# Optimization experiments

Hardware: AMD Instinct MI355X
Metric: run time of the kernel (lower is better)

Reference implementation:

```python
import jax, jax.numpy as jnp
import numpy as np

C = 384; NH = 12; HD = C // NH; MLP = int(C * 4.0)
B = 8; T = 12; N = 256; BT = B * T
EPS = 1e-6


def _ln(x):
    # LayerNorm without affine, eps=1e-6
    mu = jnp.mean(x, axis=-1, keepdims=True)
    var = jnp.mean(jnp.square(x - mu), axis=-1, keepdims=True)
    return (x - mu) / jnp.sqrt(var + EPS)


def _attention(x, wqkv, bqkv, wproj, bproj, bias=None):
    b, n, c = x.shape
    qkv = (x @ wqkv.T + bqkv).reshape(b, n, 3, NH, HD)
    q = qkv[:, :, 0].transpose(0, 2, 1, 3)  # [b,h,n,d]
    k = qkv[:, :, 1].transpose(0, 2, 1, 3)
    v = qkv[:, :, 2].transpose(0, 2, 1, 3)
    attn = jnp.einsum('bhnd,bhmd->bhnm', q, k) * (HD ** -0.5)
    if bias is not None:
        attn = attn + bias
    attn = jax.nn.softmax(attn, axis=-1)
    out = jnp.einsum('bhnm,bhmd->bhnd', attn, v).transpose(0, 2, 1, 3).reshape(b, n, c)
    return out @ wproj.T + bproj, attn


def setup_inputs() -> dict:
    key = jax.random.key(0)
    ks = jax.random.split(key, 20)
    s = 0.02
    inp = {
        'x': jax.random.normal(ks[0], (BT, N, C), jnp.float32),
        'c': jax.random.normal(ks[1], (BT, C), jnp.float32),
        'rel_pos_bias': jax.random.normal(ks[2], (1, NH, N, N), jnp.float32) * s,
        'w_adaln': jax.random.normal(ks[3], (9 * C, C), jnp.float32) * s,
        'b_adaln': jnp.zeros((9 * C,), jnp.float32),
        'wqkv_s': jax.random.normal(ks[4], (3 * C, C), jnp.float32) * s,
        'bqkv_s': jnp.zeros((3 * C,), jnp.float32),
        'wproj_s': jax.random.normal(ks[5], (C, C), jnp.float32) * s,
        'bproj_s': jnp.zeros((C,), jnp.float32),
        'wqkv_t': jax.random.normal(ks[6], (3 * C, C), jnp.float32) * s,
        'bqkv_t': jnp.zeros((3 * C,), jnp.float32),
        'wproj_t': jax.random.normal(ks[7], (C, C), jnp.float32) * s,
        'bproj_t': jnp.zeros((C,), jnp.float32),
        'w1': jax.random.normal(ks[8], (MLP, C), jnp.float32) * s,
        'b1': jnp.zeros((MLP,), jnp.float32),
        'w2': jax.random.normal(ks[9], (C, MLP), jnp.float32) * s,
        'b2': jnp.zeros((C,), jnp.float32),
        'T_pred': T,
    }
    return inp


def reference(x, c, rel_pos_bias, w_adaln, b_adaln, wqkv_s, bqkv_s, wproj_s, bproj_s,
              wqkv_t, bqkv_t, wproj_t, bproj_t, w1, b1, w2, b2, T_pred):
    mod = jax.nn.silu(c) @ w_adaln.T + b_adaln  # [BT, 9C]
    (shift_s, scale_s, gate_s, shift_t, scale_t, gate_t,
     shift_mlp, scale_mlp, gate_mlp) = jnp.split(mod, 9, axis=1)

    # spatial attention with adaLN modulate + gate
    x_mod = _ln(x) * (1 + scale_s[:, None]) + shift_s[:, None]
    x_s, attn_map = _attention(x_mod, wqkv_s, bqkv_s, wproj_s, bproj_s, bias=rel_pos_bias)
    x = x + gate_s[:, None] * x_s

    if T_pred > 1:
        bt, n, cdim = x.shape
        b = bt // T_pred
        xt = x.reshape(b, T_pred, n, cdim).transpose(0, 2, 1, 3).reshape(b * n, T_pred, cdim)
        sc = scale_t.reshape(b, 1, T_pred, cdim)
        sh = shift_t.reshape(b, 1, T_pred, cdim)
        gt = gate_t.reshape(b, 1, T_pred, cdim)
        norm_t = _ln(xt).reshape(b, n, T_pred, cdim)
        mod_t = (norm_t * (1 + sc) + sh).reshape(b * n, T_pred, cdim)
        x_t, _ = _attention(mod_t, wqkv_t, bqkv_t, wproj_t, bproj_t)
        x_t = (x_t.reshape(b, n, T_pred, cdim) * gt).transpose(0, 2, 1, 3).reshape(bt, n, cdim)
        x = x + x_t

    # gated MLP with exact (erf) GELU, matching nn.GELU default
    h = _ln(x) * (1 + scale_mlp[:, None]) + shift_mlp[:, None]
    h = jax.nn.gelu(h @ w1.T + b1, approximate=False) @ w2.T + b2
    x = x + gate_mlp[:, None] * h
    return (x, attn_map)
```

## Files before the change

### kernel.cpp

```cpp
#include <hip/hip_runtime.h>
#include <hip/hip_bf16.h>
#include <math.h>

typedef __bf16 bf16;
typedef __bf16 bf16x8 __attribute__((ext_vector_type(8)));
typedef __bf16 bf16x4 __attribute__((ext_vector_type(4)));
typedef float  f32x4  __attribute__((ext_vector_type(4)));

#define C_    384
#define NH_   12
#define HD_   32
#define MLP_  1536
#define B_    8
#define T_    12
#define N_    256
#define BT_   96
#define M_    24576
#define NINE_C 3456
#define QKV_  1152

#define GLOAD16(gptr, lptr)                                                \
  __builtin_amdgcn_global_load_lds(                                       \
      (const __attribute__((address_space(1))) void*)(gptr),              \
      (__attribute__((address_space(3))) void*)(lptr), 16, 0, 0)

__device__ __forceinline__ float wave_sum(float v) {
#pragma unroll
  for (int o = 32; o > 0; o >>= 1) v += __shfl_xor(v, o, 64);
  return v;
}

template <typename TO> __device__ __forceinline__ TO to_out(float v);
template <> __device__ __forceinline__ float to_out<float>(float v) { return v; }
template <> __device__ __forceinline__ bf16  to_out<bf16>(float v)  { return (bf16)v; }

struct F2BArgs {
  const float* src[8];
  bf16* dst[8];
  int n4[8];
};
__global__ __launch_bounds__(256) void k_f2b_all(F2BArgs a) {
  const int seg = blockIdx.y;
  const int i = blockIdx.x * 256 + threadIdx.x;
  if (i >= a.n4[seg]) return;
  if (seg == 7) {
    bf16x4 o;
    if (i < 9216) {
      float4 v = ((const float4*)a.src[7])[i];
      o[0] = (bf16)(v.x / (1.f + __expf(-v.x)));
      o[1] = (bf16)(v.y / (1.f + __expf(-v.y)));
      o[2] = (bf16)(v.z / (1.f + __expf(-v.z)));
      o[3] = (bf16)(v.w / (1.f + __expf(-v.w)));
    } else {
      o[0] = o[1] = o[2] = o[3] = (bf16)0.f;
    }
    ((bf16x4*)a.dst[7])[i] = o;
    return;
  }
  float4 v = ((const float4*)a.src[seg])[i];
  bf16x4 o;
  o[0] = (bf16)v.x; o[1] = (bf16)v.y; o[2] = (bf16)v.z; o[3] = (bf16)v.w;
  ((bf16x4*)a.dst[seg])[i] = o;
}

__global__ __launch_bounds__(256) void k_ln_mod(const float* __restrict__ x,
                                                const float* __restrict__ mod,
                                                bf16* __restrict__ out,
                                                int shift_chunk, int scale_chunk) {
  const int wave = threadIdx.x >> 6, lane = threadIdx.x & 63;
  const int r = blockIdx.x * 4 + wave;
  const float* xr = x + (size_t)r * C_;
  float2 v[3];
  float s = 0.f, ss = 0.f;
#pragma unroll
  for (int e = 0; e < 3; ++e) {
    v[e] = *(const float2*)&xr[lane * 2 + 128 * e];
    s += v[e].x + v[e].y;
    ss += v[e].x * v[e].x + v[e].y * v[e].y;
  }
  s = wave_sum(s); ss = wave_sum(ss);
  const float mean = s * (1.f / C_);
  const float var  = ss * (1.f / C_) - mean * mean;
  const float rs   = rsqrtf(var + 1e-6f);
  const int bt = r >> 8;
  const float* sh = mod + (size_t)bt * NINE_C + shift_chunk * C_;
  const float* sc = mod + (size_t)bt * NINE_C + scale_chunk * C_;
  bf16* orow = out + (size_t)r * C_;
#pragma unroll
  for (int e = 0; e < 3; ++e) {
    int cc = lane * 2 + 128 * e;
    float2 s2 = *(const float2*)&sc[cc];
    float2 h2 = *(const float2*)&sh[cc];
    union { bf16 b[2]; unsigned u; } pk;
    pk.b[0] = (bf16)((v[e].x - mean) * rs * (1.f + s2.x) + h2.x);
    pk.b[1] = (bf16)((v[e].y - mean) * rs * (1.f + s2.y) + h2.y);
    *(unsigned*)&orow[cc] = pk.u;
  }
}

template <typename TO, int EPI>
__global__ __launch_bounds__(256) void mfma_gemm(const bf16* __restrict__ A,
                                                 const bf16* __restrict__ W,
                                                 const float* __restrict__ bias,
                                                 TO* __restrict__ out,
                                                 int M, int N, int K,
                                                 const float* __restrict__ base,
                                                 const float* __restrict__ mod,
                                                 int gc, int ntx) {
  __shared__ bf16 As[128 * 64];
  __shared__ bf16 Bs[128 * 64];
  const int tid = threadIdx.x;
  const int w = tid >> 6, l = tid & 63;
  const int nwg = gridDim.x;
  const int q8 = nwg >> 3, r8 = nwg & 7;
  const int xcd = blockIdx.x & 7, idx = blockIdx.x >> 3;
  const int t = (xcd < r8 ? xcd * (q8 + 1) : r8 * (q8 + 1) + (xcd - r8) * q8) + idx;
  const int m0 = (t / ntx) * 128, n0 = (t % ntx) * 128;
  const int wr = w >> 1, wc = w & 1;
  f32x4 acc[4][4];
#pragma unroll
  for (int mi = 0; mi < 4; ++mi)
#pragma unroll
    for (int nj = 0; nj < 4; ++nj) acc[mi][nj] = (f32x4){0.f, 0.f, 0.f, 0.f};

  const int srow8 = l >> 3;
  const int c8    = l & 7;

  for (int k0 = 0; k0 < K; k0 += 64) {
#pragma unroll
    for (int i = 0; i < 4; ++i) {
      int row = w * 32 + i * 8 + srow8;
      int sc = c8 ^ (row & 7);
      GLOAD16(A + (size_t)(m0 + row) * K + k0 + sc * 8,
              (char*)As + (w * 32 + i * 8) * 128);
      GLOAD16(W + (size_t)(n0 + row) * K + k0 + sc * 8,
              (char*)Bs + (w * 32 + i * 8) * 128);
    }
    __syncthreads();
#pragma unroll
    for (int kt = 0; kt < 2; ++kt) {
      bf16x8 a[4], b[4];
      const int cc = kt * 4 + (l >> 4);
#pragma unroll
      for (int mi = 0; mi < 4; ++mi) {
        int row = wr * 64 + mi * 16 + (l & 15);
        a[mi] = *(const bf16x8*)((const char*)As + row * 128 + ((cc ^ (row & 7)) << 4));
      }
#pragma unroll
      for (int nj = 0; nj < 4; ++nj) {
        int row = wc * 64 + nj * 16 + (l & 15);
        b[nj] = *(const bf16x8*)((const char*)Bs + row * 128 + ((cc ^ (row & 7)) << 4));
      }
#pragma unroll
      for (int mi = 0; mi < 4; ++mi)
#pragma unroll
        for (int nj = 0; nj < 4; ++nj)
          acc[mi][nj] = __builtin_amdgcn_mfma_f32_16x16x32_bf16(a[mi], b[nj], acc[mi][nj], 0, 0, 0);
    }
    __syncthreads();
  }
  const int btc = m0 >> 8;
#pragma unroll
  for (int nj = 0; nj < 4; ++nj) {
    int col = n0 + wc * 64 + nj * 16 + (l & 15);
    float bv = bias[col];
    float gv = 0.f;
    if (EPI == 2 || EPI == 4) gv = mod[(size_t)btc * NINE_C + gc * C_ + col];
#pragma unroll
    for (int mi = 0; mi < 4; ++mi) {
#pragma unroll
      for (int q = 0; q < 4; ++q) {
        int rrow = m0 + wr * 64 + mi * 16 + (l >> 4) * 4 + q;
        float v = acc[mi][nj][q] + bv;
        if (EPI == 0) {
          out[(size_t)rrow * N + col] = to_out<TO>(v);
        } else if (EPI == 1) {
          v = 0.5f * v * (1.f + erff(v * 0.70710678118654752f));
          out[(size_t)rrow * N + col] = to_out<TO>(v);
        } else if (EPI == 2) {
          ((float*)out)[(size_t)rrow * N + col] =
              base[(size_t)rrow * N + col] + gv * v;
        } else {
          float o = base[(size_t)rrow * N + col] + gv * v;
          __builtin_nontemporal_store(o, &((float*)out)[(size_t)rrow * N + col]);
        }
      }
    }
  }
}

__global__ __launch_bounds__(256) void k_attn_fused(const bf16* __restrict__ qkv,
                                                    const float* __restrict__ bias,
                                                    float* __restrict__ attn,
                                                    bf16* __restrict__ out) {
  __shared__ bf16 Vt[32 * 256];
  __shared__ bf16 Pl[4][16][260];
  const int blk = blockIdx.x;
  const int bt = blk / NH_, h = blk - bt * NH_;
  const int tid = threadIdx.x;
#pragma unroll
  for (int r = 0; r < 4; ++r) {
    int id = tid + 256 * r;
    int j = id >> 2, c = id & 3;
    bf16x8 vv = *(const bf16x8*)(qkv + (size_t)(bt * N_ + j) * QKV_ + 2 * C_ + h * HD_ + c * 8);
    int kc = j >> 3, ke = j & 7;
#pragma unroll
    for (int i = 0; i < 8; ++i) {
      int d = c * 8 + i;
      *(bf16*)((char*)Vt + d * 512 + ((kc ^ (d & 7)) << 4) + ke * 2) = vv[i];
    }
  }
  const int w = tid >> 6, l = tid & 63;
  const int ln = l & 15, kg = l >> 4;
  const bf16* kbase = qkv + (size_t)bt * N_ * QKV_ + C_ + h * HD_ + kg * 8;
  bf16x8 kfr[16];
#pragma unroll
  for (int nj = 0; nj < 16; ++nj)
    kfr[nj] = *(const bf16x8*)(kbase + (size_t)(nj * 16 + ln) * QKV_);
  __syncthreads();

  const float scale = 0.17677669529663687f;
  const float* bb = bias + (size_t)h * N_ * N_;
  float* Pb = attn + (size_t)blk * N_ * N_;
  const bf16* qbase = qkv + (size_t)bt * N_ * QKV_ + h * HD_ + kg * 8;
  char* Pw = (char*)&Pl[w][0][0];

  for (int g = 0; g < 4; ++g) {
    const int i0 = w * 64 + g * 16;
    const int row = i0 + ln;
    bf16x8 aq = *(const bf16x8*)(qbase + (size_t)row * QKV_);
    f32x4 s[16];
#pragma unroll
    for (int nj = 0; nj < 16; ++nj)
      s[nj] = __builtin_amdgcn_mfma_f32_16x16x32_bf16(kfr[nj], aq, (f32x4){0.f,0.f,0.f,0.f}, 0, 0, 0);
    const float* brow = bb + (size_t)row * N_ + kg * 4;
    float v[16][4];
    float mx = -1e30f;
#pragma unroll
    for (int nj = 0; nj < 16; ++nj) {
      float4 bv = *(const float4*)(brow + nj * 16);
      v[nj][0] = s[nj][0] * scale + bv.x;
      v[nj][1] = s[nj][1] * scale + bv.y;
      v[nj][2] = s[nj][2] * scale + bv.z;
      v[nj][3] = s[nj][3] * scale + bv.w;
      mx = fmaxf(mx, fmaxf(fmaxf(v[nj][0], v[nj][1]), fmaxf(v[nj][2], v[nj][3])));
    }
    mx = fmaxf(mx, __shfl_xor(mx, 16, 64));
    mx = fmaxf(mx, __shfl_xor(mx, 32, 64));
    float sum = 0.f;
#pragma unroll
    for (int nj = 0; nj < 16; ++nj) {
      v[nj][0] = __expf(v[nj][0] - mx);
      v[nj][1] = __expf(v[nj][1] - mx);
      v[nj][2] = __expf(v[nj][2] - mx);
      v[nj][3] = __expf(v[nj][3] - mx);
      sum += (v[nj][0] + v[nj][1]) + (v[nj][2] + v[nj][3]);
    }
    sum += __shfl_xor(sum, 16, 64);
    sum += __shfl_xor(sum, 32, 64);
    const float inv = __frcp_rn(sum);
    float* prow = Pb + (size_t)row * N_ + kg * 4;
#pragma unroll
    for (int nj = 0; nj < 16; ++nj) {
      f32x4 o;
      o[0] = v[nj][0] * inv; o[1] = v[nj][1] * inv;
      o[2] = v[nj][2] * inv; o[3] = v[nj][3] * inv;
      __builtin_nontemporal_store(o, (f32x4*)(prow + nj * 16));
      bf16x4 pb;
      pb[0] = (bf16)o[0]; pb[1] = (bf16)o[1]; pb[2] = (bf16)o[2]; pb[3] = (bf16)o[3];
      *(bf16x4*)(Pw + ln * 520 + (nj * 16 + kg * 4) * 2) = pb;
    }
    f32x4 o0 = (f32x4){0.f,0.f,0.f,0.f}, o1 = (f32x4){0.f,0.f,0.f,0.f};
#pragma unroll
    for (int kt = 0; kt < 8; ++kt) {
      bf16x8 a = *(const bf16x8*)(Pw + ln * 520 + kt * 64 + kg * 16);
      int kc = kt * 4 + kg;
      bf16x8 b0 = *(const bf16x8*)((const char*)Vt + (size_t)ln * 512 + ((kc ^ (ln & 7)) << 4));
      bf16x8 b1 = *(const bf16x8*)((const char*)Vt + (size_t)(16 + ln) * 512 + ((kc ^ (ln & 7)) << 4));
      o0 = __builtin_amdgcn_mfma_f32_16x16x32_bf16(a, b0, o0, 0, 0, 0);
      o1 = __builtin_amdgcn_mfma_f32_16x16x32_bf16(a, b1, o1, 0, 0, 0);
    }
#pragma unroll
    for (int q = 0; q < 4; ++q) {
      int orow_i = i0 + kg * 4 + q;
      bf16* orow = out + (size_t)(bt * N_ + orow_i) * C_ + h * HD_;
      orow[ln]      = (bf16)o0[q];
      orow[16 + ln] = (bf16)o1[q];
    }
  }
}

__global__ __launch_bounds__(64) void k_attn_t(const bf16* __restrict__ qkv,
                                               bf16* __restrict__ out) {
  __shared__ float q[T_][HD_], k[T_][HD_], v[T_][HD_];
  const int blk = blockIdx.x;
  const int bn = blk / NH_, h = blk - bn * NH_;
  const int b = bn >> 8, n = bn & 255;
  const int tid = threadIdx.x;
  for (int idx = tid; idx < T_ * 3 * HD_; idx += 64) {
    int t = idx / 96, rem = idx - t * 96;
    int s = rem >> 5, d = rem & 31;
    const int row = (b * T_ + t) * N_ + n;
    float val = (float)qkv[(size_t)row * QKV_ + s * C_ + h * HD_ + d];
    if (s == 0) q[t][d] = val;
    else if (s == 1) k[t][d] = val;
    else v[t][d] = val;
  }
  __syncthreads();
  if (tid < T_) {
    const int i = tid;
    float sv[T_];
    float m = -1e30f;
#pragma unroll
    for (int j = 0; j < T_; ++j) {
      float s = 0.f;
#pragma unroll
      for (int d = 0; d < HD_; ++d) s += q[i][d] * k[j][d];
      s *= 0.17677669529663687f;
      sv[j] = s; m = fmaxf(m, s);
    }
    float l = 0.f;
#pragma unroll
    for (int j = 0; j < T_; ++j) { sv[j] = __expf(sv[j] - m); l += sv[j]; }
    const float inv = 1.f / l;
    float o[HD_];
#pragma unroll
    for (int d = 0; d < HD_; ++d) o[d] = 0.f;
#pragma unroll
    for (int j = 0; j < T_; ++j)
#pragma unroll
      for (int d = 0; d < HD_; ++d) o[d] += sv[j] * v[j][d];
    bf16* orow = out + (size_t)((b * T_ + i) * N_ + n) * C_ + h * HD_;
#pragma unroll
    for (int d = 0; d < HD_; ++d) orow[d] = (bf16)(o[d] * inv);
  }
}

extern "C" void kernel_launch(void* const* d_in, const int* in_sizes, int n_in,
                              void* d_out, int out_size, void* d_ws, size_t ws_size,
                              hipStream_t stream) {
  const float* x_in   = (const float*)d_in[0];
  const float* c_in   = (const float*)d_in[1];
  const float* relb   = (const float*)d_in[2];
  const float* w_ada  = (const float*)d_in[3];
  const float* b_ada  = (const float*)d_in[4];
  const float* wqkv_s = (const float*)d_in[5];
  const float* bqkv_s = (const float*)d_in[6];
  const float* wproj_s= (const float*)d_in[7];
  const float* bproj_s= (const float*)d_in[8];
  const float* wqkv_t = (const float*)d_in[9];
  const float* bqkv_t = (const float*)d_in[10];
  const float* wproj_t= (const float*)d_in[11];
  const float* bproj_t= (const float*)d_in[12];
  const float* w1     = (const float*)d_in[13];
  const float* b1     = (const float*)d_in[14];
  const float* w2     = (const float*)d_in[15];
  const float* b2     = (const float*)d_in[16];

  float* Xout = (float*)d_out;
  float* attn = (float*)d_out + (size_t)M_ * C_;

  char* ws = (char*)d_ws;
  float* mod    = (float*)ws;
  bf16*  silu_b = (bf16*)(ws + 1769472);
  bf16*  Wb     = (bf16*)(ws + 1867776);
  bf16*  Bbuf   = (bf16*)(ws + 9240576);
  bf16*  Abuf   = (bf16*)(ws + 28114944);

  bf16* wqkv_s_b  = Wb;
  bf16* wproj_s_b = Wb + 442368;
  bf16* wqkv_t_b  = Wb + 589824;
  bf16* wproj_t_b = Wb + 1032192;
  bf16* w1_b      = Wb + 1179648;
  bf16* w2_b      = Wb + 1769472;
  bf16* wada_b    = Wb + 2359296;

  F2BArgs fa;
  fa.src[0] = wqkv_s;  fa.dst[0] = wqkv_s_b;  fa.n4[0] = 110592;
  fa.src[1] = wproj_s; fa.dst[1] = wproj_s_b; fa.n4[1] = 36864;
  fa.src[2] = wqkv_t;  fa.dst[2] = wqkv_t_b;  fa.n4[2] = 110592;
  fa.src[3] = wproj_t; fa.dst[3] = wproj_t_b; fa.n4[3] = 36864;
  fa.src[4] = w1;      fa.dst[4] = w1_b;      fa.n4[4] = 147456;
  fa.src[5] = w2;      fa.dst[5] = w2_b;      fa.n4[5] = 147456;
  fa.src[6] = w_ada;   fa.dst[6] = wada_b;    fa.n4[6] = 331776;
  fa.src[7] = c_in;    fa.dst[7] = silu_b;    fa.n4[7] = 12288;
  k_f2b_all<<<dim3(1296, 8), 256, 0, stream>>>(fa);

  mfma_gemm<float, 0><<<27, 256, 0, stream>>>(
      silu_b, wada_b, b_ada, mod, 128, NINE_C, C_, nullptr, nullptr, 0, 27);

  k_ln_mod<<<M_ / 4, 256, 0, stream>>>(x_in, mod, Bbuf, 0, 1);
  mfma_gemm<bf16, 0><<<(QKV_/128)*(M_/128), 256, 0, stream>>>(
      Bbuf, wqkv_s_b, bqkv_s, Abuf, M_, QKV_, C_, nullptr, nullptr, 0, QKV_/128);
  k_attn_fused<<<BT_ * NH_, 256, 0, stream>>>(Abuf, relb, attn, Bbuf);
  mfma_gemm<float, 2><<<(C_/128)*(M_/128), 256, 0, stream>>>(
      Bbuf, wproj_s_b, bproj_s, (float*)Xout, M_, C_, C_, x_in, mod, 2, C_/128);

  k_ln_mod<<<M_ / 4, 256, 0, stream>>>(Xout, mod, Bbuf, 3, 4);
  mfma_gemm<bf16, 0><<<(QKV_/128)*(M_/128), 256, 0, stream>>>(
      Bbuf, wqkv_t_b, bqkv_t, Abuf, M_, QKV_, C_, nullptr, nullptr, 0, QKV_/128);
  k_attn_t<<<B_ * N_ * NH_, 64, 0, stream>>>(Abuf, Bbuf);
  mfma_gemm<float, 2><<<(C_/128)*(M_/128), 256, 0, stream>>>(
      Bbuf, wproj_t_b, bproj_t, (float*)Xout, M_, C_, C_, Xout, mod, 5, C_/128);

  k_ln_mod<<<M_ / 4, 256, 0, stream>>>(Xout, mod, Bbuf, 6, 7);
  mfma_gemm<bf16, 1><<<(MLP_/128)*(M_/128), 256, 0, stream>>>(
      Bbuf, w1_b, b1, Abuf, M_, MLP_, C_, nullptr, nullptr, 0, MLP_/128);
  mfma_gemm<float, 4><<<(C_/128)*(M_/128), 256, 0, stream>>>(
      Abuf, w2_b, b2, (float*)Xout, M_, C_, MLP_, Xout, mod, 8, C_/128);
}
```

Before: 446.2 us.

## Restructure temporal attention to one block per token with all heads, compact f2b grid

Temporal attention now launches one 256-thread block per (batch, spatial position). The block loads the full QKV rows for all 12 timesteps into LDS with 16-byte vector loads, and 144 threads handle all 12 heads at once. Before, each block handled a single head with 64 threads, only 12 of them active, and used scalar loads. Outputs are written as packed bf16 pairs. The weight conversion kernel also switches from a padded 2D grid to a compact 1D grid with per-segment block offsets, which removes many idle blocks. The attention change trades occupancy and LDS bank patterns for far fewer, wider blocks and coalesced loads.

```diff
diff --git a/kernel.cpp b/kernel.cpp
--- a/kernel.cpp
+++ b/kernel.cpp
@@ -38,10 +38,14 @@
   const float* src[8];
   bf16* dst[8];
   int n4[8];
+  int start[9];
 };
 __global__ __launch_bounds__(256) void k_f2b_all(F2BArgs a) {
-  const int seg = blockIdx.y;
-  const int i = blockIdx.x * 256 + threadIdx.x;
+  const int blk = blockIdx.x;
+  int seg = 0;
+#pragma unroll
+  for (int s = 1; s < 8; ++s) seg += (blk >= a.start[s]);
+  const int i = (blk - a.start[seg]) * 256 + threadIdx.x;
   if (i >= a.n4[seg]) return;
   if (seg == 7) {
     bf16x4 o;
@@ -290,32 +294,32 @@
   }
 }
 
-__global__ __launch_bounds__(64) void k_attn_t(const bf16* __restrict__ qkv,
-                                               bf16* __restrict__ out) {
-  __shared__ float q[T_][HD_], k[T_][HD_], v[T_][HD_];
-  const int blk = blockIdx.x;
-  const int bn = blk / NH_, h = blk - bn * NH_;
+#define TROW 1168
+__global__ __launch_bounds__(256) void k_attn_t(const bf16* __restrict__ qkv,
+                                                bf16* __restrict__ out) {
+  __shared__ bf16 S[T_ * TROW];
+  const int bn = blockIdx.x;
   const int b = bn >> 8, n = bn & 255;
   const int tid = threadIdx.x;
-  for (int idx = tid; idx < T_ * 3 * HD_; idx += 64) {
-    int t = idx / 96, rem = idx - t * 96;
-    int s = rem >> 5, d = rem & 31;
-    const int row = (b * T_ + t) * N_ + n;
-    float val = (float)qkv[(size_t)row * QKV_ + s * C_ + h * HD_ + d];
-    if (s == 0) q[t][d] = val;
-    else if (s == 1) k[t][d] = val;
-    else v[t][d] = val;
+  for (int c = tid; c < T_ * 144; c += 256) {
+    int t = c / 144, off = (c - t * 144) * 8;
+    bf16x8 vv = *(const bf16x8*)(qkv + (size_t)((b * T_ + t) * N_ + n) * QKV_ + off);
+    *(bf16x8*)&S[t * TROW + off] = vv;
   }
   __syncthreads();
-  if (tid < T_) {
-    const int i = tid;
+  if (tid < 144) {
+    const int h = tid / 12, i = tid - h * 12;
+    const int qo = h * HD_, ko = C_ + h * HD_, vo = 2 * C_ + h * HD_;
+    float q[HD_];
+#pragma unroll
+    for (int d = 0; d < HD_; ++d) q[d] = (float)S[i * TROW + qo + d];
     float sv[T_];
     float m = -1e30f;
 #pragma unroll
     for (int j = 0; j < T_; ++j) {
       float s = 0.f;
 #pragma unroll
-      for (int d = 0; d < HD_; ++d) s += q[i][d] * k[j][d];
+      for (int d = 0; d < HD_; ++d) s += q[d] * (float)S[j * TROW + ko + d];
       s *= 0.17677669529663687f;
       sv[j] = s; m = fmaxf(m, s);
     }
@@ -327,12 +331,19 @@
 #pragma unroll
     for (int d = 0; d < HD_; ++d) o[d] = 0.f;
 #pragma unroll
-    for (int j = 0; j < T_; ++j)
-#pragma unroll
-      for (int d = 0; d < HD_; ++d) o[d] += sv[j] * v[j][d];
+    for (int j = 0; j < T_; ++j) {
+      float p = sv[j];
+#pragma unroll
+      for (int d = 0; d < HD_; ++d) o[d] += p * (float)S[j * TROW + vo + d];
+    }
     bf16* orow = out + (size_t)((b * T_ + i) * N_ + n) * C_ + h * HD_;
 #pragma unroll
-    for (int d = 0; d < HD_; ++d) orow[d] = (bf16)(o[d] * inv);
+    for (int d = 0; d < HD_; d += 2) {
+      union { bf16 bb[2]; unsigned u; } pk;
+      pk.bb[0] = (bf16)(o[d] * inv);
+      pk.bb[1] = (bf16)(o[d + 1] * inv);
+      *(unsigned*)&orow[d] = pk.u;
+    }
   }
 }
 
@@ -384,7 +395,13 @@
   fa.src[5] = w2;      fa.dst[5] = w2_b;      fa.n4[5] = 147456;
   fa.src[6] = w_ada;   fa.dst[6] = wada_b;    fa.n4[6] = 331776;
   fa.src[7] = c_in;    fa.dst[7] = silu_b;    fa.n4[7] = 12288;
-  k_f2b_all<<<dim3(1296, 8), 256, 0, stream>>>(fa);
+  int total_blk = 0;
+  for (int s = 0; s < 8; ++s) {
+    fa.start[s] = total_blk;
+    total_blk += (fa.n4[s] + 255) / 256;
+  }
+  fa.start[8] = total_blk;
+  k_f2b_all<<<total_blk, 256, 0, stream>>>(fa);
 
   mfma_gemm<float, 0><<<27, 256, 0, stream>>>(
       silu_b, wada_b, b_ada, mod, 128, NINE_C, C_, nullptr, nullptr, 0, 27);
@@ -399,7 +416,7 @@
   k_ln_mod<<<M_ / 4, 256, 0, stream>>>(Xout, mod, Bbuf, 3, 4);
   mfma_gemm<bf16, 0><<<(QKV_/128)*(M_/128), 256, 0, stream>>>(
       Bbuf, wqkv_t_b, bqkv_t, Abuf, M_, QKV_, C_, nullptr, nullptr, 0, QKV_/128);
-  k_attn_t<<<B_ * N_ * NH_, 64, 0, stream>>>(Abuf, Bbuf);
+  k_attn_t<<<B_ * N_, 256, 0, stream>>>(Abuf, Bbuf);
   mfma_gemm<float, 2><<<(C_/128)*(M_/128), 256, 0, stream>>>(
       Bbuf, wproj_t_b, bproj_t, (float*)Xout, M_, C_, C_, Xout, mod, 5, C_/128);
 
```

After: 434.9 us. 1.03x faster.
